# Optimization experiments

Measured on AMD Instinct MI355X. Metric: run time of the kernel, lower is better.

The kernel has to match this reference:

```python
import jax, jax.numpy as jnp
import numpy as np

BSZ, NGEN, NCLS, SEQ, G = 64, 128, 30, 2048, 16  # G = gold triples per example (fixed)

POS_NAMES = ["sub_start_logits", "sub_end_logits", "obj_start_logits", "obj_end_logits",
             "aspect_start_logits", "aspect_end_logits", "opinion_start_logits", "opinion_end_logits"]
GOLD_NAMES = ["gold_sub_start", "gold_sub_end", "gold_obj_start", "gold_obj_end",
              "gold_aspect_start", "gold_aspect_end", "gold_opinion_start", "gold_opinion_end"]


def _lsa(C):
    """Exact rectangular linear sum assignment (Jonker-Volgenant shortest augmenting
    path), equivalent to scipy.optimize.linear_sum_assignment. Returns (row_ind, col_ind)."""
    C = np.asarray(C, dtype=np.float64)
    transposed = C.shape[0] > C.shape[1]
    if transposed:
        C = C.T
    n, m = C.shape
    u = np.zeros(n + 1)
    v = np.zeros(m + 1)
    p = np.zeros(m + 1, dtype=np.int64)    # p[j] = row (1-based) assigned to column j
    way = np.zeros(m + 1, dtype=np.int64)
    for i in range(1, n + 1):
        p[0] = i
        j0 = 0
        minv = np.full(m + 1, np.inf)
        used = np.zeros(m + 1, dtype=bool)
        while True:
            used[j0] = True
            i0 = p[j0]
            cur = C[i0 - 1] - u[i0] - v[1:]
            better = (~used[1:]) & (cur < minv[1:])
            minv[1:] = np.where(better, cur, minv[1:])
            way[1:] = np.where(better, j0, way[1:])
            cand = np.where(~used[1:], minv[1:], np.inf)
            j1 = int(np.argmin(cand)) + 1
            delta = cand[j1 - 1]
            for j in np.where(used)[0]:
                u[p[j]] += delta
                v[j] -= delta
            minv[~used] -= delta
            j0 = j1
            if p[j0] == 0:
                break
        while j0:
            j1 = way[j0]
            p[j0] = p[j1]
            j0 = j1
    col = np.full(n, -1, dtype=np.int64)
    for j in range(1, m + 1):
        if p[j]:
            col[p[j] - 1] = j - 1
    row = np.arange(n, dtype=np.int64)
    if transposed:
        order = np.argsort(col)
        return col[order], row[order]
    return row, col


def setup_inputs() -> dict:
    key = jax.random.key(0)
    ks = jax.random.split(key, 18)
    d = {"pred_rel_logits": jax.random.normal(ks[0], (BSZ, NGEN, NCLS), jnp.float32)}
    for i, name in enumerate(POS_NAMES):
        d[name] = jax.random.normal(ks[1 + i], (BSZ, NGEN, SEQ), jnp.float32)
    d["gold_rel"] = jax.random.randint(ks[9], (BSZ * G,), 0, NCLS)
    for i, name in enumerate(GOLD_NAMES):
        d[name] = jax.random.randint(ks[10 + i], (BSZ * G,), 0, SEQ)
    return d


def _cost(pred_rel_logits, sub_start_logits, sub_end_logits, obj_start_logits, obj_end_logits,
          aspect_start_logits, aspect_end_logits, opinion_start_logits, opinion_end_logits,
          gold_rel, gold_sub_start, gold_sub_end, gold_obj_start, gold_obj_end,
          gold_aspect_start, gold_aspect_end, gold_opinion_start, gold_opinion_end):
    bsz, ngen = pred_rel_logits.shape[:2]
    sm = lambda x: jax.nn.softmax(x.reshape(bsz * ngen, -1), axis=-1)
    # cost: [bsz*ngen, total_gold], matcher == 'avg'
    cost = -(sm(pred_rel_logits)[:, gold_rel]
             + sm(sub_start_logits)[:, gold_sub_start] + sm(sub_end_logits)[:, gold_sub_end]
             + sm(obj_start_logits)[:, gold_obj_start] + sm(obj_end_logits)[:, gold_obj_end]
             + sm(aspect_start_logits)[:, gold_aspect_start] + sm(aspect_end_logits)[:, gold_aspect_end]
             + sm(opinion_start_logits)[:, gold_opinion_start] + sm(opinion_end_logits)[:, gold_opinion_end])
    return cost.reshape(bsz, ngen, -1)


_cost_jit = jax.jit(_cost)


def reference(pred_rel_logits, sub_start_logits, sub_end_logits, obj_start_logits, obj_end_logits,
              aspect_start_logits, aspect_end_logits, opinion_start_logits, opinion_end_logits,
              gold_rel, gold_sub_start, gold_sub_end, gold_obj_start, gold_obj_end,
              gold_aspect_start, gold_aspect_end, gold_opinion_start, gold_opinion_end):
    cost = _cost_jit(pred_rel_logits, sub_start_logits, sub_end_logits, obj_start_logits,
                     obj_end_logits, aspect_start_logits, aspect_end_logits,
                     opinion_start_logits, opinion_end_logits,
                     gold_rel, gold_sub_start, gold_sub_end, gold_obj_start, gold_obj_end,
                     gold_aspect_start, gold_aspect_end, gold_opinion_start, gold_opinion_end)
    cnp = np.asarray(cost)
    rows = np.zeros((BSZ, G), dtype=np.int64)
    cols = np.zeros((BSZ, G), dtype=np.int64)
    # per-example assignment on the example's own block of gold columns (mirrors cost.split)
    for b in range(BSZ):
        r, c = _lsa(cnp[b, :, b * G:(b + 1) * G])
        rows[b], cols[b] = r, c
    return cost, jnp.asarray(rows), jnp.asarray(cols)
```

## Files before the change

kernel.cpp:

```cpp
#include <hip/hip_runtime.h>
#include <math.h>

#define BSZ   64
#define NGEN  128
#define NCLS  30
#define SEQ   2048
#define G     16
#define NQ    (BSZ * NGEN)
#define TG    (BSZ * G)
#define COST_ELEMS ((size_t)NQ * TG)
#define OFF_ROWS COST_ELEMS
#define OFF_COLS (COST_ELEMS + TG)

__global__ __launch_bounds__(1024, 8) void cost_kernel(
    const float* __restrict__ rel,
    const float* __restrict__ p0, const float* __restrict__ p1,
    const float* __restrict__ p2, const float* __restrict__ p3,
    const float* __restrict__ p4, const float* __restrict__ p5,
    const float* __restrict__ p6, const float* __restrict__ p7,
    const int* __restrict__ grel,
    const int* __restrict__ g0, const int* __restrict__ g1,
    const int* __restrict__ g2, const int* __restrict__ g3,
    const int* __restrict__ g4, const int* __restrict__ g5,
    const int* __restrict__ g6, const int* __restrict__ g7,
    float* __restrict__ out)
{
    __shared__ float ex[8][SEQ];
    __shared__ float relex[32];
    __shared__ float spart[16];
    __shared__ float srel;

    const int tid  = threadIdx.x;
    const int q    = blockIdx.x;
    const int lane = tid & 63;
    const int wv   = tid >> 6;
    const int kloc = tid >> 7;
    const int r    = tid & 127;

    const int j0_ = g0[tid], j1_ = g1[tid], j2_ = g2[tid], j3_ = g3[tid];
    const int j4_ = g4[tid], j5_ = g5[tid], j6_ = g6[tid], j7_ = g7[tid];
    const int jr_ = grel[tid];

    const float* pk =
        (kloc == 0) ? p0 : (kloc == 1) ? p1 : (kloc == 2) ? p2 :
        (kloc == 3) ? p3 : (kloc == 4) ? p4 : (kloc == 5) ? p5 :
        (kloc == 6) ? p6 : p7;

    const float4* row4 = (const float4*)(pk + (size_t)q * SEQ);
    float4 x0 = row4[r];
    float4 x1 = row4[r + 128];
    float4 x2 = row4[r + 256];
    float4 x3 = row4[r + 384];

    float4 e0, e1, e2, e3;
    e0.x = __expf(x0.x); e0.y = __expf(x0.y); e0.z = __expf(x0.z); e0.w = __expf(x0.w);
    e1.x = __expf(x1.x); e1.y = __expf(x1.y); e1.z = __expf(x1.z); e1.w = __expf(x1.w);
    e2.x = __expf(x2.x); e2.y = __expf(x2.y); e2.z = __expf(x2.z); e2.w = __expf(x2.w);
    e3.x = __expf(x3.x); e3.y = __expf(x3.y); e3.z = __expf(x3.z); e3.w = __expf(x3.w);

    float s = (((e0.x + e0.y) + (e0.z + e0.w)) + ((e1.x + e1.y) + (e1.z + e1.w)))
            + (((e2.x + e2.y) + (e2.z + e2.w)) + ((e3.x + e3.y) + (e3.z + e3.w)));
    #pragma unroll
    for (int off = 32; off; off >>= 1) s += __shfl_xor(s, off);

    float4* exk = (float4*)ex[kloc];
    exk[r]       = e0;
    exk[r + 128] = e1;
    exk[r + 256] = e2;
    exk[r + 384] = e3;
    if (lane == 0) spart[wv] = s;

    if (wv == 0) {
        float e = (lane < NCLS) ? __expf(rel[(size_t)q * NCLS + lane]) : 0.f;
        if (lane < 32) relex[lane] = e;
        float s2 = e;
        #pragma unroll
        for (int off = 32; off; off >>= 1) s2 += __shfl_xor(s2, off);
        if (lane == 0) srel = s2;
    }
    __syncthreads();

    const float d0 = spart[0]  + spart[1];
    const float d1 = spart[2]  + spart[3];
    const float d2 = spart[4]  + spart[5];
    const float d3 = spart[6]  + spart[7];
    const float d4 = spart[8]  + spart[9];
    const float d5 = spart[10] + spart[11];
    const float d6 = spart[12] + spart[13];
    const float d7 = spart[14] + spart[15];

    float acc = relex[jr_] * __builtin_amdgcn_rcpf(srel);
    acc = fmaf(ex[0][j0_], __builtin_amdgcn_rcpf(d0), acc);
    acc = fmaf(ex[1][j1_], __builtin_amdgcn_rcpf(d1), acc);
    acc = fmaf(ex[2][j2_], __builtin_amdgcn_rcpf(d2), acc);
    acc = fmaf(ex[3][j3_], __builtin_amdgcn_rcpf(d3), acc);
    acc = fmaf(ex[4][j4_], __builtin_amdgcn_rcpf(d4), acc);
    acc = fmaf(ex[5][j5_], __builtin_amdgcn_rcpf(d5), acc);
    acc = fmaf(ex[6][j6_], __builtin_amdgcn_rcpf(d6), acc);
    acc = fmaf(ex[7][j7_], __builtin_amdgcn_rcpf(d7), acc);

    out[(size_t)q * TG + tid] = -acc;
}

__global__ __launch_bounds__(64) void lsa_kernel(const float* __restrict__ cost,
                                                 float* __restrict__ out)
{
    const int b    = blockIdx.x;
    const int lane = threadIdx.x;

    __shared__ float C[G][NGEN];
    __shared__ int   colArr[G];

    for (int e = lane; e < G * NGEN; e += 64) {
        int j = e >> 4, i = e & (G - 1);
        C[i][j] = cost[((size_t)(b * NGEN + j)) * TG + b * G + i];
    }
    __syncthreads();

    const double INFD = (double)INFINITY;

    double u_r = 0.0;
    double v0 = 0.0, v1 = 0.0;
    int    p0c = 0, p1c = 0;
    int    pcol0 = 0;

    for (int i = 1; i <= G; ++i) {
        pcol0 = i;
        double minv0 = INFD, minv1 = INFD;
        int way0 = 0, way1 = 0;
        bool used0 = false, used1 = false;
        bool inTree = false;
        int j0 = 0;

        while (true) {
            int i0;
            if (j0 == 0) {
                i0 = pcol0;
            } else {
                int ow = (j0 - 1) & 63, c = (j0 - 1) >> 6;
                if (lane == ow) { if (c == 0) used0 = true; else used1 = true; }
                int pv = (c == 0) ? p0c : p1c;
                i0 = __shfl(pv, ow);
            }
            if (lane == i0) inTree = true;
            double ui0 = __shfl(u_r, i0);

            float c0f = C[i0 - 1][lane];
            float c1f = C[i0 - 1][lane + 64];
            if (!used0) {
                double cur = (double)c0f - ui0 - v0;
                if (cur < minv0) { minv0 = cur; way0 = j0; }
            }
            if (!used1) {
                double cur = (double)c1f - ui0 - v1;
                if (cur < minv1) { minv1 = cur; way1 = j0; }
            }

            double bv = INFD; int bj = 1 << 30;
            if (!used0) { bv = minv0; bj = 1 + lane; }
            if (!used1 && minv1 < bv) { bv = minv1; bj = 65 + lane; }
            #pragma unroll
            for (int off = 32; off; off >>= 1) {
                double ov = __shfl_xor(bv, off);
                int    oj = __shfl_xor(bj, off);
                if (ov < bv || (ov == bv && oj < bj)) { bv = ov; bj = oj; }
            }
            const double delta = bv;
            const int    j1    = bj;

            if (inTree) u_r += delta;
            if (used0) v0 -= delta; else minv0 -= delta;
            if (used1) v1 -= delta; else minv1 -= delta;

            j0 = j1;
            int ow = (j0 - 1) & 63, c = (j0 - 1) >> 6;
            int pv = (c == 0) ? p0c : p1c;
            if (__shfl(pv, ow) == 0) break;
        }

        while (j0) {
            int ow = (j0 - 1) & 63, c = (j0 - 1) >> 6;
            int wv_ = (c == 0) ? way0 : way1;
            int j1 = __shfl(wv_, ow);
            int pv;
            if (j1 == 0) {
                pv = pcol0;
            } else {
                int ow1 = (j1 - 1) & 63, c1 = (j1 - 1) >> 6;
                int t2 = (c1 == 0) ? p0c : p1c;
                pv = __shfl(t2, ow1);
            }
            if (lane == ow) { if (c == 0) p0c = pv; else p1c = pv; }
            j0 = j1;
        }
    }

    if (p0c != 0) colArr[p0c - 1] = lane;
    if (p1c != 0) colArr[p1c - 1] = lane + 64;
    __syncthreads();
    if (lane < G) {
        int ci = colArr[lane];
        int rank = 0;
        #pragma unroll
        for (int j = 0; j < G; ++j) rank += (colArr[j] < ci) ? 1 : 0;
        out[OFF_ROWS + b * G + rank] = (float)ci;
        out[OFF_COLS + b * G + rank] = (float)lane;
    }
}

extern "C" void kernel_launch(void* const* d_in, const int* in_sizes, int n_in,
                              void* d_out, int out_size, void* d_ws, size_t ws_size,
                              hipStream_t stream) {
    const float* rel = (const float*)d_in[0];
    const float* p0  = (const float*)d_in[1];
    const float* p1  = (const float*)d_in[2];
    const float* p2  = (const float*)d_in[3];
    const float* p3  = (const float*)d_in[4];
    const float* p4  = (const float*)d_in[5];
    const float* p5  = (const float*)d_in[6];
    const float* p6  = (const float*)d_in[7];
    const float* p7  = (const float*)d_in[8];
    const int* grel = (const int*)d_in[9];
    const int* g0 = (const int*)d_in[10];
    const int* g1 = (const int*)d_in[11];
    const int* g2 = (const int*)d_in[12];
    const int* g3 = (const int*)d_in[13];
    const int* g4 = (const int*)d_in[14];
    const int* g5 = (const int*)d_in[15];
    const int* g6 = (const int*)d_in[16];
    const int* g7 = (const int*)d_in[17];
    float* out = (float*)d_out;

    cost_kernel<<<NQ, 1024, 0, stream>>>(rel, p0, p1, p2, p3, p4, p5, p6, p7,
                                         grel, g0, g1, g2, g3, g4, g5, g6, g7, out);
    lsa_kernel<<<BSZ, 64, 0, stream>>>(out, out);
}
```

Before: 492.6 us.

## Process multiple queries per block with register prefetch of next row

Each cost block now handles 16 queries in a loop instead of one, so the gold index loads and block launch overhead are amortized. The next query's logits rows are loaded into registers while the current query's softmax and gather run, overlapping global loads with compute. It uses raw s_barrier with explicit lgkmcnt waits in place of __syncthreads. The grid shrinks to 512 blocks, which may reduce occupancy and latency hiding across CUs.

After: 507.0 us. 2.9% more time.

```diff
diff --git a/kernel.cpp b/kernel.cpp
--- a/kernel.cpp
+++ b/kernel.cpp
@@ -8,6 +8,8 @@
 #define G     16
 #define NQ    (BSZ * NGEN)
 #define TG    (BSZ * G)
+#define QPB   16
+#define NBLK  (NQ / QPB)
 #define COST_ELEMS ((size_t)NQ * TG)
 #define OFF_ROWS COST_ELEMS
 #define OFF_COLS (COST_ELEMS + TG)
@@ -31,7 +33,6 @@
     __shared__ float srel;
 
     const int tid  = threadIdx.x;
-    const int q    = blockIdx.x;
     const int lane = tid & 63;
     const int wv   = tid >> 6;
     const int kloc = tid >> 7;
@@ -46,60 +47,84 @@
         (kloc == 3) ? p3 : (kloc == 4) ? p4 : (kloc == 5) ? p5 :
         (kloc == 6) ? p6 : p7;
 
-    const float4* row4 = (const float4*)(pk + (size_t)q * SEQ);
-    float4 x0 = row4[r];
-    float4 x1 = row4[r + 128];
-    float4 x2 = row4[r + 256];
-    float4 x3 = row4[r + 384];
-
-    float4 e0, e1, e2, e3;
-    e0.x = __expf(x0.x); e0.y = __expf(x0.y); e0.z = __expf(x0.z); e0.w = __expf(x0.w);
-    e1.x = __expf(x1.x); e1.y = __expf(x1.y); e1.z = __expf(x1.z); e1.w = __expf(x1.w);
-    e2.x = __expf(x2.x); e2.y = __expf(x2.y); e2.z = __expf(x2.z); e2.w = __expf(x2.w);
-    e3.x = __expf(x3.x); e3.y = __expf(x3.y); e3.z = __expf(x3.z); e3.w = __expf(x3.w);
-
-    float s = (((e0.x + e0.y) + (e0.z + e0.w)) + ((e1.x + e1.y) + (e1.z + e1.w)))
-            + (((e2.x + e2.y) + (e2.z + e2.w)) + ((e3.x + e3.y) + (e3.z + e3.w)));
-    #pragma unroll
-    for (int off = 32; off; off >>= 1) s += __shfl_xor(s, off);
-
-    float4* exk = (float4*)ex[kloc];
-    exk[r]       = e0;
-    exk[r + 128] = e1;
-    exk[r + 256] = e2;
-    exk[r + 384] = e3;
-    if (lane == 0) spart[wv] = s;
-
-    if (wv == 0) {
-        float e = (lane < NCLS) ? __expf(rel[(size_t)q * NCLS + lane]) : 0.f;
-        if (lane < 32) relex[lane] = e;
-        float s2 = e;
+    const int qbase = blockIdx.x * QPB;
+
+    {
+        const float4* row4 = (const float4*)(pk + (size_t)qbase * SEQ);
+    }
+    const float4* row4p = (const float4*)(pk + (size_t)qbase * SEQ);
+    float4 x0 = row4p[r];
+    float4 x1 = row4p[r + 128];
+    float4 x2 = row4p[r + 256];
+    float4 x3 = row4p[r + 384];
+    float relx = (wv == 0 && lane < NCLS) ? rel[(size_t)qbase * NCLS + lane] : 0.f;
+
+    for (int it = 0; it < QPB; ++it) {
+        const int qq = qbase + it;
+
+        float4 e0, e1, e2, e3;
+        e0.x = __expf(x0.x); e0.y = __expf(x0.y); e0.z = __expf(x0.z); e0.w = __expf(x0.w);
+        e1.x = __expf(x1.x); e1.y = __expf(x1.y); e1.z = __expf(x1.z); e1.w = __expf(x1.w);
+        e2.x = __expf(x2.x); e2.y = __expf(x2.y); e2.z = __expf(x2.z); e2.w = __expf(x2.w);
+        e3.x = __expf(x3.x); e3.y = __expf(x3.y); e3.z = __expf(x3.z); e3.w = __expf(x3.w);
+
+        float s = (((e0.x + e0.y) + (e0.z + e0.w)) + ((e1.x + e1.y) + (e1.z + e1.w)))
+                + (((e2.x + e2.y) + (e2.z + e2.w)) + ((e3.x + e3.y) + (e3.z + e3.w)));
         #pragma unroll
-        for (int off = 32; off; off >>= 1) s2 += __shfl_xor(s2, off);
-        if (lane == 0) srel = s2;
-    }
-    __syncthreads();
-
-    const float d0 = spart[0]  + spart[1];
-    const float d1 = spart[2]  + spart[3];
-    const float d2 = spart[4]  + spart[5];
-    const float d3 = spart[6]  + spart[7];
-    const float d4 = spart[8]  + spart[9];
-    const float d5 = spart[10] + spart[11];
-    const float d6 = spart[12] + spart[13];
-    const float d7 = spart[14] + spart[15];
-
-    float acc = relex[jr_] * __builtin_amdgcn_rcpf(srel);
-    acc = fmaf(ex[0][j0_], __builtin_amdgcn_rcpf(d0), acc);
-    acc = fmaf(ex[1][j1_], __builtin_amdgcn_rcpf(d1), acc);
-    acc = fmaf(ex[2][j2_], __builtin_amdgcn_rcpf(d2), acc);
-    acc = fmaf(ex[3][j3_], __builtin_amdgcn_rcpf(d3), acc);
-    acc = fmaf(ex[4][j4_], __builtin_amdgcn_rcpf(d4), acc);
-    acc = fmaf(ex[5][j5_], __builtin_amdgcn_rcpf(d5), acc);
-    acc = fmaf(ex[6][j6_], __builtin_amdgcn_rcpf(d6), acc);
-    acc = fmaf(ex[7][j7_], __builtin_amdgcn_rcpf(d7), acc);
-
-    out[(size_t)q * TG + tid] = -acc;
+        for (int off = 32; off; off >>= 1) s += __shfl_xor(s, off);
+
+        float4* exk = (float4*)ex[kloc];
+        exk[r]       = e0;
+        exk[r + 128] = e1;
+        exk[r + 256] = e2;
+        exk[r + 384] = e3;
+        if (lane == 0) spart[wv] = s;
+
+        if (wv == 0) {
+            float e = (lane < NCLS) ? __expf(relx) : 0.f;
+            if (lane < 32) relex[lane] = e;
+            float s2 = e;
+            #pragma unroll
+            for (int off = 32; off; off >>= 1) s2 += __shfl_xor(s2, off);
+            if (lane == 0) srel = s2;
+        }
+
+        if (it + 1 < QPB) {
+            const float4* nrow = (const float4*)(pk + (size_t)(qq + 1) * SEQ);
+            x0 = nrow[r];
+            x1 = nrow[r + 128];
+            x2 = nrow[r + 256];
+            x3 = nrow[r + 384];
+            if (wv == 0 && lane < NCLS) relx = rel[(size_t)(qq + 1) * NCLS + lane];
+        }
+
+        asm volatile("s_waitcnt lgkmcnt(0)" ::: "memory");
+        __builtin_amdgcn_s_barrier();
+
+        const float d0 = spart[0]  + spart[1];
+        const float d1 = spart[2]  + spart[3];
+        const float d2 = spart[4]  + spart[5];
+        const float d3 = spart[6]  + spart[7];
+        const float d4 = spart[8]  + spart[9];
+        const float d5 = spart[10] + spart[11];
+        const float d6 = spart[12] + spart[13];
+        const float d7 = spart[14] + spart[15];
+
+        float acc = relex[jr_] * __builtin_amdgcn_rcpf(srel);
+        acc = fmaf(ex[0][j0_], __builtin_amdgcn_rcpf(d0), acc);
+        acc = fmaf(ex[1][j1_], __builtin_amdgcn_rcpf(d1), acc);
+        acc = fmaf(ex[2][j2_], __builtin_amdgcn_rcpf(d2), acc);
+        acc = fmaf(ex[3][j3_], __builtin_amdgcn_rcpf(d3), acc);
+        acc = fmaf(ex[4][j4_], __builtin_amdgcn_rcpf(d4), acc);
+        acc = fmaf(ex[5][j5_], __builtin_amdgcn_rcpf(d5), acc);
+        acc = fmaf(ex[6][j6_], __builtin_amdgcn_rcpf(d6), acc);
+        acc = fmaf(ex[7][j7_], __builtin_amdgcn_rcpf(d7), acc);
+
+        out[(size_t)qq * TG + tid] = -acc;
+
+        asm volatile("s_waitcnt lgkmcnt(0)" ::: "memory");
+        __builtin_amdgcn_s_barrier();
+    }
 }
 
 __global__ __launch_bounds__(64) void lsa_kernel(const float* __restrict__ cost,
@@ -231,7 +256,7 @@
     const int* g7 = (const int*)d_in[17];
     float* out = (float*)d_out;
 
-    cost_kernel<<<NQ, 1024, 0, stream>>>(rel, p0, p1, p2, p3, p4, p5, p6, p7,
-                                         grel, g0, g1, g2, g3, g4, g5, g6, g7, out);
+    cost_kernel<<<NBLK, 1024, 0, stream>>>(rel, p0, p1, p2, p3, p4, p5, p6, p7,
+                                           grel, g0, g1, g2, g3, g4, g5, g6, g7, out);
     lsa_kernel<<<BSZ, 64, 0, stream>>>(out, out);
 }
```
